# Kernel optimization log

Hardware: AMD Instinct MI355X
Metric: run time of the kernel (lower is better)

## Reference

```python
import jax, jax.numpy as jnp
import numpy as np

B, C, Q, D = 64, 1024, 256, 128
NEG = -1e30  # VERY_NEGATIVE_NUMBER


def setup_inputs() -> dict:
    key = jax.random.key(0)
    k1, k2, k3, k4, k5, k6 = jax.random.split(key, 6)
    return {
        "x_cont": jax.random.normal(k1, (B, C, D), dtype=jnp.float32),
        "x_ques": jax.random.normal(k2, (B, Q, D), dtype=jnp.float32),
        "c_mask": jnp.ones((B, C), dtype=jnp.float32),
        "q_mask": jnp.ones((B, Q), dtype=jnp.float32),
        "W0": jax.random.uniform(k3, (D, 1), jnp.float32, -0.1, 0.1),
        "W1": jax.random.uniform(k4, (D, 1), jnp.float32, -0.1, 0.1),
        "W2": jax.random.uniform(k5, (1, 1, D), jnp.float32, -0.1, 0.1),
        "bias": jnp.zeros((1,), dtype=jnp.float32),
    }


def reference(x_cont, x_ques, c_mask, q_mask, W0, W1, W2, bias):
    # Trilinear similarity S[b,c,q] = x_cont.W0 + x_ques.W1 + (x_cont*W2).x_ques^T + bias
    s0 = x_cont @ W0                                   # [B,C,1]
    s1 = jnp.swapaxes(x_ques @ W1, 1, 2)               # [B,1,Q]
    s2 = jnp.einsum('bcd,bqd->bcq', x_cont * W2, x_ques)  # [B,C,Q]
    S = s0 + s1 + s2 + bias                            # [B,C,Q]

    qm = q_mask[:, None, :]                            # [B,1,Q]
    cm = c_mask[:, :, None]                            # [B,C,1]
    S_ = jax.nn.softmax(S + NEG * (1.0 - qm), axis=-1)           # row softmax [B,C,Q]
    S_T = jnp.swapaxes(jax.nn.softmax(S + NEG * (1.0 - cm), axis=1), 1, 2)  # [B,Q,C]

    c2q = S_ @ x_ques                                  # [B,C,D]
    q2c = (S_ @ S_T) @ x_cont                          # [B,C,D]
    return jnp.concatenate([x_cont, c2q, x_cont * c2q, x_cont * q2c], axis=-1)
```

## Files before the change

### kernel.cpp

```cpp
#include <hip/hip_runtime.h>
#include <math.h>

#define BB 64
#define CC 1024
#define QQ 256
#define DD 128
#define NEGV (-1.0e30f)

typedef short bf8 __attribute__((ext_vector_type(8)));
typedef short bf4 __attribute__((ext_vector_type(4)));
typedef float f4v __attribute__((ext_vector_type(4)));

__device__ __forceinline__ short f2bf(float f) {
    unsigned u = __builtin_bit_cast(unsigned, f);
    u += 0x7FFFu + ((u >> 16) & 1u);
    return (short)(u >> 16);
}
__device__ __forceinline__ float bf2f(short s) {
    unsigned u = ((unsigned)(unsigned short)s) << 16;
    return __builtin_bit_cast(float, u);
}

__global__ __launch_bounds__(256, 2) void k0_all(
        const float* __restrict__ xc, const float* __restrict__ xq,
        const float* __restrict__ W0, const float* __restrict__ W1,
        const float* __restrict__ W2,
        const float* __restrict__ c_mask, const float* __restrict__ q_mask,
        float* __restrict__ s0m, float* __restrict__ s1m,
        short* __restrict__ xc_bf, short* __restrict__ xqw_bf,
        short* __restrict__ xcT_bf, short* __restrict__ xqT_bf) {
    __shared__ float tile[64][129];
    int bid = blockIdx.x;
    const float *src, *W, *mask;
    float* sm; short *rm, *tr;
    int b, tl, R; bool use2;
    if (bid < 1024) {
        b = ((bid >> 7) << 3) | (bid & 7); tl = (bid >> 3) & 15; R = CC;
        src = xc; W = W0; mask = c_mask; sm = s0m; rm = xc_bf; tr = xcT_bf; use2 = false;
    } else {
        int q = bid - 1024;
        b = ((q >> 5) << 3) | (q & 7); tl = (q >> 3) & 3; R = QQ;
        src = xq; W = W1; mask = q_mask; sm = s1m; rm = xqw_bf; tr = xqT_bf; use2 = true;
    }
    int r0 = tl * 64;
    int t = threadIdx.x;
    int c4 = t & 31, rr = t >> 5;
    float4 wv = ((const float4*)W)[c4];
    float4 sc4 = use2 ? ((const float4*)W2)[c4] : make_float4(1.f, 1.f, 1.f, 1.f);
    const float* sb = src + ((size_t)b * R + r0) * DD;
    #pragma unroll
    for (int p = 0; p < 8; ++p) {
        int row = rr + p * 8;
        float4 g = *(const float4*)&sb[(size_t)row * DD + c4 * 4];
        bf4 o;
        o[0] = f2bf(g.x * sc4.x); o[1] = f2bf(g.y * sc4.y);
        o[2] = f2bf(g.z * sc4.z); o[3] = f2bf(g.w * sc4.w);
        *(bf4*)&rm[((size_t)(b * R + r0 + row)) * DD + c4 * 4] = o;
        float part = g.x * wv.x + g.y * wv.y + g.z * wv.z + g.w * wv.w;
        #pragma unroll
        for (int off = 1; off < 32; off <<= 1) part += __shfl_xor(part, off, 64);
        if ((t & 31) == 0)
            sm[(size_t)b * R + r0 + row] =
                part + NEGV * (1.0f - mask[(size_t)b * R + r0 + row]);
        tile[row][c4 * 4 + 0] = g.x; tile[row][c4 * 4 + 1] = g.y;
        tile[row][c4 * 4 + 2] = g.z; tile[row][c4 * 4 + 3] = g.w;
    }
    __syncthreads();
    int rj = (t & 7) * 8;
    #pragma unroll
    for (int pp = 0; pp < 4; ++pp) {
        int d = pp * 32 + (t >> 3);
        bf8 o;
        #pragma unroll
        for (int j = 0; j < 8; ++j) o[j] = f2bf(tile[rj + j][d]);
        *(bf8*)&tr[((size_t)(b * DD + d)) * R + r0 + rj] = o;
    }
}

#define SCP 1032
#define S2P 264
#define XTP 72

#define K1_LDA(G, S, CT)                                                 \
    {                                                                    \
        const short* ar_ = abase + (size_t)(CT) * 64 * DD;               \
        G[0] = *(const bf8*)&ar_[0];  G[1] = *(const bf8*)&ar_[32];      \
        G[2] = *(const bf8*)&ar_[64]; G[3] = *(const bf8*)&ar_[96];      \
        S = *(const f4v*)&s0base[(CT) * 64];                             \
    }

#define K1_STEPA(G, S, CT)                                                            \
    {                                                                                 \
        f4v acc = {0.f, 0.f, 0.f, 0.f};                                               \
        acc = __builtin_amdgcn_mfma_f32_16x16x32_bf16(G[0], bq[0], acc, 0, 0, 0);     \
        acc = __builtin_amdgcn_mfma_f32_16x16x32_bf16(G[1], bq[1], acc, 0, 0, 0);     \
        acc = __builtin_amdgcn_mfma_f32_16x16x32_bf16(G[2], bq[2], acc, 0, 0, 0);     \
        acc = __builtin_amdgcn_mfma_f32_16x16x32_bf16(G[3], bq[3], acc, 0, 0, 0);     \
        bf4 ov;                                                                       \
        ov[0] = f2bf(acc[0] + S[0]); ov[1] = f2bf(acc[1] + S[1]);                     \
        ov[2] = f2bf(acc[2] + S[2]); ov[3] = f2bf(acc[3] + S[3]);                     \
        *(bf4*)&sc[l16][(CT) * 64 + w * 16 + quad * 4] = ov;                          \
        if ((CT) + 4 < 16) K1_LDA(G, S, (CT) + 4);                                    \
    }

#define K1_STG(GS, NXT)                                                  \
    {                                                                    \
        *(bf8*)&xct[dr][c8 * 8] = GS[0];                                 \
        *(bf8*)&xct[dr + 32][c8 * 8] = GS[1];                            \
        *(bf8*)&xct[dr + 64][c8 * 8] = GS[2];                            \
        *(bf8*)&xct[dr + 96][c8 * 8] = GS[3];                            \
        if ((NXT) < 16) {                                                \
            GS[0] = *(const bf8*)&tbase[(NXT) * 64];                     \
            GS[1] = *(const bf8*)&tbase[(size_t)32 * CC + (NXT) * 64];   \
            GS[2] = *(const bf8*)&tbase[(size_t)64 * CC + (NXT) * 64];   \
            GS[3] = *(const bf8*)&tbase[(size_t)96 * CC + (NXT) * 64];   \
        }                                                                \
    }

#define K1_CSTEP(CT)                                                               \
    {                                                                              \
        bf8 a0 = *(const bf8*)&sc[l16][(CT) * 64 + quad * 8];                      \
        bf8 b0 = *(const bf8*)&xct[w * 32 + l16][quad * 8];                        \
        acc0 = __builtin_amdgcn_mfma_f32_16x16x32_bf16(a0, b0, acc0, 0, 0, 0);     \
        bf8 b1 = *(const bf8*)&xct[w * 32 + 16 + l16][quad * 8];                   \
        acc1 = __builtin_amdgcn_mfma_f32_16x16x32_bf16(a0, b1, acc1, 0, 0, 0);     \
        bf8 a1 = *(const bf8*)&sc[l16][(CT) * 64 + 32 + quad * 8];                 \
        bf8 b2 = *(const bf8*)&xct[w * 32 + l16][32 + quad * 8];                   \
        acc0 = __builtin_amdgcn_mfma_f32_16x16x32_bf16(a1, b2, acc0, 0, 0, 0);     \
        bf8 b3 = *(const bf8*)&xct[w * 32 + 16 + l16][32 + quad * 8];              \
        acc1 = __builtin_amdgcn_mfma_f32_16x16x32_bf16(a1, b3, acc1, 0, 0, 0);     \
    }

__global__ __launch_bounds__(256, 3) void k1_colsm(
        const short* __restrict__ xc_bf, const short* __restrict__ xcT_bf,
        const short* __restrict__ xqw_bf, const float* __restrict__ s0m,
        short* __restrict__ AT) {
    __shared__ __align__(16) short sc[16][SCP];
    __shared__ __align__(16) short xct[DD][XTP];
    __shared__ float invl[16];

    int bid = blockIdx.x;
    int qt = (bid >> 3) & 15;
    int b = ((bid >> 7) << 3) | (bid & 7);
    int q0 = qt * 16;
    int t = threadIdx.x, w = t >> 6, l = t & 63;
    int quad = l >> 4, l16 = l & 15;

    bf8 bq[4];
    {
        const short* qp = &xqw_bf[(size_t)(b * QQ + q0 + l16) * DD + quad * 8];
        #pragma unroll
        for (int ks = 0; ks < 4; ++ks) bq[ks] = *(const bf8*)&qp[ks * 32];
    }

    const short* abase = &xc_bf[(size_t)(b * CC + w * 16 + l16) * DD + quad * 8];
    const float* s0base = &s0m[b * CC + w * 16 + quad * 4];
    bf8 gA[4], gB[4], gC[4], gD[4];
    f4v sA, sB, sC, sD;
    K1_LDA(gA, sA, 0); K1_LDA(gB, sB, 1); K1_LDA(gC, sC, 2); K1_LDA(gD, sD, 3);
    #pragma unroll
    for (int c4t = 0; c4t < 16; c4t += 4) {
        K1_STEPA(gA, sA, c4t + 0);
        K1_STEPA(gB, sB, c4t + 1);
        K1_STEPA(gC, sC, c4t + 2);
        K1_STEPA(gD, sD, c4t + 3);
    }

    int c8 = t & 7, dr = t >> 3;
    const short* tbase = &xcT_bf[(size_t)(b * DD + dr) * CC + c8 * 8];
    bf8 gS0[4], gS1[4];
    gS0[0] = *(const bf8*)&tbase[0];
    gS0[1] = *(const bf8*)&tbase[(size_t)32 * CC];
    gS0[2] = *(const bf8*)&tbase[(size_t)64 * CC];
    gS0[3] = *(const bf8*)&tbase[(size_t)96 * CC];
    gS1[0] = *(const bf8*)&tbase[64];
    gS1[1] = *(const bf8*)&tbase[(size_t)32 * CC + 64];
    gS1[2] = *(const bf8*)&tbase[(size_t)64 * CC + 64];
    gS1[3] = *(const bf8*)&tbase[(size_t)96 * CC + 64];

    __syncthreads();

    {
        int q = t >> 4, k = t & 15;
        bf8 v[8];
        #pragma unroll
        for (int j = 0; j < 8; ++j) v[j] = *(const bf8*)&sc[q][k * 8 + j * 128];
        float m = -3.0e38f;
        #pragma unroll
        for (int j = 0; j < 8; ++j)
            #pragma unroll
            for (int e = 0; e < 8; ++e) m = fmaxf(m, bf2f(v[j][e]));
        #pragma unroll
        for (int off = 1; off < 16; off <<= 1) m = fmaxf(m, __shfl_xor(m, off, 64));
        float sum = 0.f;
        #pragma unroll
        for (int j = 0; j < 8; ++j) {
            bf8 o;
            #pragma unroll
            for (int e = 0; e < 8; ++e) {
                float ex = __expf(bf2f(v[j][e]) - m);
                sum += ex;
                o[e] = f2bf(ex);
            }
            *(bf8*)&sc[q][k * 8 + j * 128] = o;
        }
        #pragma unroll
        for (int off = 1; off < 16; off <<= 1) sum += __shfl_xor(sum, off, 64);
        if (k == 0) invl[q] = 1.0f / sum;
    }
    __syncthreads();

    f4v acc0 = {0.f, 0.f, 0.f, 0.f}, acc1 = {0.f, 0.f, 0.f, 0.f};
    #pragma unroll
    for (int ct = 0; ct < 16; ct += 2) {
        K1_STG(gS0, ct + 2);
        __syncthreads();
        K1_CSTEP(ct);
        __syncthreads();
        K1_STG(gS1, ct + 3);
        __syncthreads();
        K1_CSTEP(ct + 1);
        __syncthreads();
    }
    {
        bf4 o0, o1;
        #pragma unroll
        for (int r = 0; r < 4; ++r) {
            float il = invl[quad * 4 + r];
            o0[r] = f2bf(acc0[r] * il);
            o1[r] = f2bf(acc1[r] * il);
        }
        int d0 = w * 32 + l16;
        *(bf4*)&AT[(size_t)(b * DD + d0) * QQ + q0 + quad * 4] = o0;
        *(bf4*)&AT[(size_t)(b * DD + d0 + 16) * QQ + q0 + quad * 4] = o1;
    }
}

#define K2_LDA(G, CT)                                                    \
    {                                                                    \
        const short* ar_ = abase + (size_t)(CT) * 64 * DD;               \
        G[0] = *(const bf8*)&ar_[0];  G[1] = *(const bf8*)&ar_[32];      \
        G[2] = *(const bf8*)&ar_[64]; G[3] = *(const bf8*)&ar_[96];     \
    }

#define K2_STEP1(G, SV, QT)                                                           \
    {                                                                                 \
        f4v acc0 = {0.f, 0.f, 0.f, 0.f}, acc1 = {0.f, 0.f, 0.f, 0.f};                 \
        acc0 = __builtin_amdgcn_mfma_f32_16x16x32_bf16(G[0], bc0[0], acc0, 0, 0, 0);  \
        acc1 = __builtin_amdgcn_mfma_f32_16x16x32_bf16(G[0], bc1[0], acc1, 0, 0, 0);  \
        acc0 = __builtin_amdgcn_mfma_f32_16x16x32_bf16(G[1], bc0[1], acc0, 0, 0, 0);  \
        acc1 = __builtin_amdgcn_mfma_f32_16x16x32_bf16(G[1], bc1[1], acc1, 0, 0, 0);  \
        acc0 = __builtin_amdgcn_mfma_f32_16x16x32_bf16(G[2], bc0[2], acc0, 0, 0, 0);  \
        acc1 = __builtin_amdgcn_mfma_f32_16x16x32_bf16(G[2], bc1[2], acc1, 0, 0, 0);  \
        acc0 = __builtin_amdgcn_mfma_f32_16x16x32_bf16(G[3], bc0[3], acc0, 0, 0, 0);  \
        acc1 = __builtin_amdgcn_mfma_f32_16x16x32_bf16(G[3], bc1[3], acc1, 0, 0, 0);  \
        int qbase_ = (QT) * 64 + w * 16 + quad * 4;                                   \
        bf4 o0, o1;                                                                   \
        o0[0] = f2bf(acc0[0] + SV[0]); o0[1] = f2bf(acc0[1] + SV[1]);                 \
        o0[2] = f2bf(acc0[2] + SV[2]); o0[3] = f2bf(acc0[3] + SV[3]);                 \
        o1[0] = f2bf(acc1[0] + SV[0]); o1[1] = f2bf(acc1[1] + SV[1]);                 \
        o1[2] = f2bf(acc1[2] + SV[2]); o1[3] = f2bf(acc1[3] + SV[3]);                 \
        *(bf4*)&sc2[l16][qbase_] = o0;                                                \
        *(bf4*)&sc2[16 + l16][qbase_] = o1;                                           \
    }

#define K2_SRC(NT) ((NT) < 4 ? (qtb + (size_t)(NT) * 64) : (atb + (size_t)((NT) - 4) * 64))

#define K2_STG(GS, NT)                                                   \
    {                                                                    \
        *(bf8*)&tT[dr][c8 * 8] = GS[0];                                  \
        *(bf8*)&tT[dr + 32][c8 * 8] = GS[1];                             \
        *(bf8*)&tT[dr + 64][c8 * 8] = GS[2];                             \
        *(bf8*)&tT[dr + 96][c8 * 8] = GS[3];                             \
        if ((NT) < 8) {                                                  \
            const short* gs_ = K2_SRC(NT);                               \
            GS[0] = *(const bf8*)&gs_[0];                                \
            GS[1] = *(const bf8*)&gs_[(size_t)32 * QQ];                  \
            GS[2] = *(const bf8*)&gs_[(size_t)64 * QQ];                  \
            GS[3] = *(const bf8*)&gs_[(size_t)96 * QQ];                  \
        }                                                                \
    }

#define K2_CSTEP(TL)                                                                   \
    {                                                                                  \
        int qoff_ = ((TL) & 3) * 64;                                                   \
        _Pragma("unroll")                                                              \
        for (int ks = 0; ks < 2; ++ks) {                                               \
            bf8 a0 = *(const bf8*)&sc2[l16][qoff_ + ks * 32 + quad * 8];               \
            bf8 a1 = *(const bf8*)&sc2[16 + l16][qoff_ + ks * 32 + quad * 8];          \
            bf8 b0 = *(const bf8*)&tT[w * 32 + l16][ks * 32 + quad * 8];               \
            bf8 b1 = *(const bf8*)&tT[w * 32 + 16 + l16][ks * 32 + quad * 8];          \
            if ((TL) < 4) {                                                            \
                ac[0][0] = __builtin_amdgcn_mfma_f32_16x16x32_bf16(a0, b0, ac[0][0], 0, 0, 0); \
                ac[0][1] = __builtin_amdgcn_mfma_f32_16x16x32_bf16(a0, b1, ac[0][1], 0, 0, 0); \
                ac[1][0] = __builtin_amdgcn_mfma_f32_16x16x32_bf16(a1, b0, ac[1][0], 0, 0, 0); \
                ac[1][1] = __builtin_amdgcn_mfma_f32_16x16x32_bf16(a1, b1, ac[1][1], 0, 0, 0); \
            } else {                                                                   \
                aq[0][0] = __builtin_amdgcn_mfma_f32_16x16x32_bf16(a0, b0, aq[0][0], 0, 0, 0); \
                aq[0][1] = __builtin_amdgcn_mfma_f32_16x16x32_bf16(a0, b1, aq[0][1], 0, 0, 0); \
                aq[1][0] = __builtin_amdgcn_mfma_f32_16x16x32_bf16(a1, b0, aq[1][0], 0, 0, 0); \
                aq[1][1] = __builtin_amdgcn_mfma_f32_16x16x32_bf16(a1, b1, aq[1][1], 0, 0, 0); \
            }                                                                          \
        }                                                                              \
    }

__global__ __launch_bounds__(256, 4) void k2_rowsm(
        const float* __restrict__ xc, const short* __restrict__ xc_bf,
        const short* __restrict__ xqw_bf, const short* __restrict__ xqT_bf,
        const short* __restrict__ AT, const float* __restrict__ s1m,
        float* __restrict__ out) {
    __shared__ __align__(16) short sc2[32][S2P];
    __shared__ __align__(16) short tT[DD][XTP];
    __shared__ float invl2[32];

    int bid = blockIdx.x;
    int cb = (bid >> 3) & 31;
    int b = ((bid >> 8) << 3) | (bid & 7);
    int c0g = cb * 32;
    int t = threadIdx.x, w = t >> 6, l = t & 63;
    int quad = l >> 4, l16 = l & 15;

    bf8 bc0[4], bc1[4];
    {
        const short* p0 = &xc_bf[(size_t)(b * CC + c0g + l16) * DD + quad * 8];
        const short* p1 = p0 + 16 * DD;
        #pragma unroll
        for (int ks = 0; ks < 4; ++ks) {
            bc0[ks] = *(const bf8*)&p0[ks * 32];
            bc1[ks] = *(const bf8*)&p1[ks * 32];
        }
    }

    const short* abase = &xqw_bf[(size_t)(b * QQ + w * 16 + l16) * DD + quad * 8];
    const float* s1base = &s1m[b * QQ + w * 16 + quad * 4];
    f4v sv0 = *(const f4v*)&s1base[0];
    f4v sv1 = *(const f4v*)&s1base[64];
    f4v sv2 = *(const f4v*)&s1base[128];
    f4v sv3 = *(const f4v*)&s1base[192];
    bf8 gA[4], gB[4];
    K2_LDA(gA, 0); K2_LDA(gB, 1);
    K2_STEP1(gA, sv0, 0); K2_LDA(gA, 2);
    K2_STEP1(gB, sv1, 1); K2_LDA(gB, 3);
    K2_STEP1(gA, sv2, 2);
    K2_STEP1(gB, sv3, 3);

    int c8 = t & 7, dr = t >> 3;
    const short* qtb = &xqT_bf[(size_t)(b * DD + dr) * QQ + c8 * 8];
    const short* atb = &AT[(size_t)(b * DD + dr) * QQ + c8 * 8];
    bf8 gS0[4], gS1[4];
    gS0[0] = *(const bf8*)&qtb[0];
    gS0[1] = *(const bf8*)&qtb[(size_t)32 * QQ];
    gS0[2] = *(const bf8*)&qtb[(size_t)64 * QQ];
    gS0[3] = *(const bf8*)&qtb[(size_t)96 * QQ];
    gS1[0] = *(const bf8*)&qtb[64];
    gS1[1] = *(const bf8*)&qtb[(size_t)32 * QQ + 64];
    gS1[2] = *(const bf8*)&qtb[(size_t)64 * QQ + 64];
    gS1[3] = *(const bf8*)&qtb[(size_t)96 * QQ + 64];

    __syncthreads();

    {
        int c = t >> 3, k = t & 7;
        bf8 v[4];
        #pragma unroll
        for (int j = 0; j < 4; ++j) v[j] = *(const bf8*)&sc2[c][k * 8 + j * 64];
        float m = -3.0e38f;
        #pragma unroll
        for (int j = 0; j < 4; ++j)
            #pragma unroll
            for (int e = 0; e < 8; ++e) m = fmaxf(m, bf2f(v[j][e]));
        #pragma unroll
        for (int off = 1; off < 8; off <<= 1) m = fmaxf(m, __shfl_xor(m, off, 64));
        float sum = 0.f;
        #pragma unroll
        for (int j = 0; j < 4; ++j) {
            bf8 o;
            #pragma unroll
            for (int e = 0; e < 8; ++e) {
                float ex = __expf(bf2f(v[j][e]) - m);
                sum += ex;
                o[e] = f2bf(ex);
            }
            *(bf8*)&sc2[c][k * 8 + j * 64] = o;
        }
        #pragma unroll
        for (int off = 1; off < 8; off <<= 1) sum += __shfl_xor(sum, off, 64);
        if (k == 0) invl2[c] = 1.0f / sum;
    }
    __syncthreads();

    f4v ac[2][2], aq[2][2];
    f4v zz = {0.f, 0.f, 0.f, 0.f};
    #pragma unroll
    for (int i = 0; i < 2; ++i)
        #pragma unroll
        for (int j = 0; j < 2; ++j) { ac[i][j] = zz; aq[i][j] = zz; }
    #pragma unroll
    for (int tl = 0; tl < 8; tl += 2) {
        K2_STG(gS0, tl + 2);
        __syncthreads();
        K2_CSTEP(tl);
        __syncthreads();
        K2_STG(gS1, tl + 3);
        __syncthreads();
        K2_CSTEP(tl + 1);
        __syncthreads();
    }

    #pragma unroll
    for (int cf = 0; cf < 2; ++cf)
        #pragma unroll
        for (int r = 0; r < 4; ++r) {
            int cl = cf * 16 + quad * 4 + r;
            int c = c0g + cl;
            float il = invl2[cl];
            const float* xrow = xc + (size_t)(b * CC + c) * DD;
            float* orow = out + (size_t)(b * CC + c) * (4 * DD);
            #pragma unroll
            for (int df = 0; df < 2; ++df) {
                int d = w * 32 + df * 16 + l16;
                float xv = xrow[d];
                float c2v = ac[cf][df][r] * il;
                float q2v = aq[cf][df][r] * il;
                orow[d] = xv;
                orow[DD + d] = c2v;
                orow[2 * DD + d] = xv * c2v;
                orow[3 * DD + d] = xv * q2v;
            }
        }
}

extern "C" void kernel_launch(void* const* d_in, const int* in_sizes, int n_in,
                              void* d_out, int out_size, void* d_ws, size_t ws_size,
                              hipStream_t stream) {
    const float* x_cont = (const float*)d_in[0];
    const float* x_ques = (const float*)d_in[1];
    const float* c_mask = (const float*)d_in[2];
    const float* q_mask = (const float*)d_in[3];
    const float* W0     = (const float*)d_in[4];
    const float* W1     = (const float*)d_in[5];
    const float* W2     = (const float*)d_in[6];
    float* out = (float*)d_out;

    char* ws = (char*)d_ws;
    float* s0m    = (float*)ws;  ws += (size_t)BB * CC * 4;
    float* s1m    = (float*)ws;  ws += (size_t)BB * QQ * 4;
    short* xc_bf  = (short*)ws;  ws += (size_t)BB * CC * DD * 2;
    short* xqw_bf = (short*)ws;  ws += (size_t)BB * QQ * DD * 2;
    short* xcT_bf = (short*)ws;  ws += (size_t)BB * CC * DD * 2;
    short* xqT_bf = (short*)ws;  ws += (size_t)BB * QQ * DD * 2;
    short* AT     = (short*)ws;

    k0_all<<<BB * 16 + BB * 4, 256, 0, stream>>>(x_cont, x_ques, W0, W1, W2,
                                                 c_mask, q_mask, s0m, s1m,
                                                 xc_bf, xqw_bf, xcT_bf, xqT_bf);
    k1_colsm<<<BB * 16, 256, 0, stream>>>(xc_bf, xcT_bf, xqw_bf, s0m, AT);
    k2_rowsm<<<BB * 32, 256, 0, stream>>>(x_cont, xc_bf, xqw_bf, xqT_bf, AT, s1m, out);
}
```

Baseline: 261.2 us.

## Use per-wave LDS staging slices and coalesce output stores through LDS

The shared transposed tiles in both kernels are split into per-wave slices of 32 rows, and each wave loads only the rows it later consumes. This removes all block-wide barriers from the inner MFMA loops and relies on in-order LDS access within a wave. The k2 epilogue now stages the c2q and q2c accumulators into reused shared memory, then writes the output with contiguous float4 loads and stores instead of scattered scalar writes. The cost is two extra barriers and an LDS round trip in the epilogue, plus reliance on the reused buffers being large enough.

```diff
diff --git a/kernel.cpp b/kernel.cpp
--- a/kernel.cpp
+++ b/kernel.cpp
@@ -103,31 +103,33 @@
         if ((CT) + 4 < 16) K1_LDA(G, S, (CT) + 4);                                    \
     }
 
-#define K1_STG(GS, NXT)                                                  \
-    {                                                                    \
-        *(bf8*)&xct[dr][c8 * 8] = GS[0];                                 \
-        *(bf8*)&xct[dr + 32][c8 * 8] = GS[1];                            \
-        *(bf8*)&xct[dr + 64][c8 * 8] = GS[2];                            \
-        *(bf8*)&xct[dr + 96][c8 * 8] = GS[3];                            \
-        if ((NXT) < 16) {                                                \
-            GS[0] = *(const bf8*)&tbase[(NXT) * 64];                     \
-            GS[1] = *(const bf8*)&tbase[(size_t)32 * CC + (NXT) * 64];   \
-            GS[2] = *(const bf8*)&tbase[(size_t)64 * CC + (NXT) * 64];   \
-            GS[3] = *(const bf8*)&tbase[(size_t)96 * CC + (NXT) * 64];   \
-        }                                                                \
+#define K1_LDS2(G, CT)                                                   \
+    {                                                                    \
+        G[0] = *(const bf8*)&tbase[(CT) * 64];                           \
+        G[1] = *(const bf8*)&tbase[(size_t)8 * CC + (CT) * 64];          \
+        G[2] = *(const bf8*)&tbase[(size_t)16 * CC + (CT) * 64];         \
+        G[3] = *(const bf8*)&tbase[(size_t)24 * CC + (CT) * 64];         \
+    }
+
+#define K1_WRS2(G)                                                       \
+    {                                                                    \
+        *(bf8*)&xct[w][sr][c8l * 8] = G[0];                              \
+        *(bf8*)&xct[w][sr + 8][c8l * 8] = G[1];                          \
+        *(bf8*)&xct[w][sr + 16][c8l * 8] = G[2];                         \
+        *(bf8*)&xct[w][sr + 24][c8l * 8] = G[3];                         \
     }
 
 #define K1_CSTEP(CT)                                                               \
     {                                                                              \
         bf8 a0 = *(const bf8*)&sc[l16][(CT) * 64 + quad * 8];                      \
-        bf8 b0 = *(const bf8*)&xct[w * 32 + l16][quad * 8];                        \
+        bf8 b0 = *(const bf8*)&xct[w][l16][quad * 8];                              \
         acc0 = __builtin_amdgcn_mfma_f32_16x16x32_bf16(a0, b0, acc0, 0, 0, 0);     \
-        bf8 b1 = *(const bf8*)&xct[w * 32 + 16 + l16][quad * 8];                   \
+        bf8 b1 = *(const bf8*)&xct[w][16 + l16][quad * 8];                         \
         acc1 = __builtin_amdgcn_mfma_f32_16x16x32_bf16(a0, b1, acc1, 0, 0, 0);     \
         bf8 a1 = *(const bf8*)&sc[l16][(CT) * 64 + 32 + quad * 8];                 \
-        bf8 b2 = *(const bf8*)&xct[w * 32 + l16][32 + quad * 8];                   \
+        bf8 b2 = *(const bf8*)&xct[w][l16][32 + quad * 8];                         \
         acc0 = __builtin_amdgcn_mfma_f32_16x16x32_bf16(a1, b2, acc0, 0, 0, 0);     \
-        bf8 b3 = *(const bf8*)&xct[w * 32 + 16 + l16][32 + quad * 8];              \
+        bf8 b3 = *(const bf8*)&xct[w][16 + l16][32 + quad * 8];                    \
         acc1 = __builtin_amdgcn_mfma_f32_16x16x32_bf16(a1, b3, acc1, 0, 0, 0);     \
     }
 
@@ -136,7 +138,7 @@
         const short* __restrict__ xqw_bf, const float* __restrict__ s0m,
         short* __restrict__ AT) {
     __shared__ __align__(16) short sc[16][SCP];
-    __shared__ __align__(16) short xct[DD][XTP];
+    __shared__ __align__(16) short xct[4][32][XTP];
     __shared__ float invl[16];
 
     int bid = blockIdx.x;
@@ -166,17 +168,11 @@
         K1_STEPA(gD, sD, c4t + 3);
     }
 
-    int c8 = t & 7, dr = t >> 3;
-    const short* tbase = &xcT_bf[(size_t)(b * DD + dr) * CC + c8 * 8];
+    int c8l = l & 7, sr = l >> 3;
+    const short* tbase = &xcT_bf[(size_t)(b * DD + w * 32 + sr) * CC + c8l * 8];
     bf8 gS0[4], gS1[4];
-    gS0[0] = *(const bf8*)&tbase[0];
-    gS0[1] = *(const bf8*)&tbase[(size_t)32 * CC];
-    gS0[2] = *(const bf8*)&tbase[(size_t)64 * CC];
-    gS0[3] = *(const bf8*)&tbase[(size_t)96 * CC];
-    gS1[0] = *(const bf8*)&tbase[64];
-    gS1[1] = *(const bf8*)&tbase[(size_t)32 * CC + 64];
-    gS1[2] = *(const bf8*)&tbase[(size_t)64 * CC + 64];
-    gS1[3] = *(const bf8*)&tbase[(size_t)96 * CC + 64];
+    K1_LDS2(gS0, 0);
+    K1_LDS2(gS1, 1);
 
     __syncthreads();
 
@@ -211,16 +207,20 @@
     __syncthreads();
 
     f4v acc0 = {0.f, 0.f, 0.f, 0.f}, acc1 = {0.f, 0.f, 0.f, 0.f};
-    #pragma unroll
-    for (int ct = 0; ct < 16; ct += 2) {
-        K1_STG(gS0, ct + 2);
-        __syncthreads();
+    K1_WRS2(gS0);
+    K1_LDS2(gS0, 2);
+    #pragma unroll
+    for (int ct = 0; ct < 16; ++ct) {
         K1_CSTEP(ct);
-        __syncthreads();
-        K1_STG(gS1, ct + 3);
-        __syncthreads();
-        K1_CSTEP(ct + 1);
-        __syncthreads();
+        if (ct < 15) {
+            if ((ct & 1) == 0) {
+                K1_WRS2(gS1);
+                if (ct + 3 < 16) K1_LDS2(gS1, ct + 3);
+            } else {
+                K1_WRS2(gS0);
+                if (ct + 3 < 16) K1_LDS2(gS0, ct + 3);
+            }
+        }
     }
     {
         bf4 o0, o1;
@@ -240,7 +240,7 @@
     {                                                                    \
         const short* ar_ = abase + (size_t)(CT) * 64 * DD;               \
         G[0] = *(const bf8*)&ar_[0];  G[1] = *(const bf8*)&ar_[32];      \
-        G[2] = *(const bf8*)&ar_[64]; G[3] = *(const bf8*)&ar_[96];     \
+        G[2] = *(const bf8*)&ar_[64]; G[3] = *(const bf8*)&ar_[96];      \
     }
 
 #define K2_STEP1(G, SV, QT)                                                           \
@@ -264,21 +264,23 @@
         *(bf4*)&sc2[16 + l16][qbase_] = o1;                                           \
     }
 
-#define K2_SRC(NT) ((NT) < 4 ? (qtb + (size_t)(NT) * 64) : (atb + (size_t)((NT) - 4) * 64))
-
-#define K2_STG(GS, NT)                                                   \
-    {                                                                    \
-        *(bf8*)&tT[dr][c8 * 8] = GS[0];                                  \
-        *(bf8*)&tT[dr + 32][c8 * 8] = GS[1];                             \
-        *(bf8*)&tT[dr + 64][c8 * 8] = GS[2];                             \
-        *(bf8*)&tT[dr + 96][c8 * 8] = GS[3];                             \
-        if ((NT) < 8) {                                                  \
-            const short* gs_ = K2_SRC(NT);                               \
-            GS[0] = *(const bf8*)&gs_[0];                                \
-            GS[1] = *(const bf8*)&gs_[(size_t)32 * QQ];                  \
-            GS[2] = *(const bf8*)&gs_[(size_t)64 * QQ];                  \
-            GS[3] = *(const bf8*)&gs_[(size_t)96 * QQ];                  \
-        }                                                                \
+#define K2_SRC(NT) ((NT) < 4 ? (qtb + (size_t)((NT) & 3) * 64) : (atb + (size_t)((NT) - 4) * 64))
+
+#define K2_LDS2(G, NT)                                                   \
+    {                                                                    \
+        const short* gs_ = K2_SRC(NT);                                   \
+        G[0] = *(const bf8*)&gs_[0];                                     \
+        G[1] = *(const bf8*)&gs_[(size_t)8 * QQ];                        \
+        G[2] = *(const bf8*)&gs_[(size_t)16 * QQ];                       \
+        G[3] = *(const bf8*)&gs_[(size_t)24 * QQ];                       \
+    }
+
+#define K2_WRS2(G)                                                       \
+    {                                                                    \
+        *(bf8*)&tT[w][sr][c8l * 8] = G[0];                               \
+        *(bf8*)&tT[w][sr + 8][c8l * 8] = G[1];                           \
+        *(bf8*)&tT[w][sr + 16][c8l * 8] = G[2];                          \
+        *(bf8*)&tT[w][sr + 24][c8l * 8] = G[3];                          \
     }
 
 #define K2_CSTEP(TL)                                                                   \
@@ -288,8 +290,8 @@
         for (int ks = 0; ks < 2; ++ks) {                                               \
             bf8 a0 = *(const bf8*)&sc2[l16][qoff_ + ks * 32 + quad * 8];               \
             bf8 a1 = *(const bf8*)&sc2[16 + l16][qoff_ + ks * 32 + quad * 8];          \
-            bf8 b0 = *(const bf8*)&tT[w * 32 + l16][ks * 32 + quad * 8];               \
-            bf8 b1 = *(const bf8*)&tT[w * 32 + 16 + l16][ks * 32 + quad * 8];          \
+            bf8 b0 = *(const bf8*)&tT[w][l16][ks * 32 + quad * 8];                     \
+            bf8 b1 = *(const bf8*)&tT[w][16 + l16][ks * 32 + quad * 8];                \
             if ((TL) < 4) {                                                            \
                 ac[0][0] = __builtin_amdgcn_mfma_f32_16x16x32_bf16(a0, b0, ac[0][0], 0, 0, 0); \
                 ac[0][1] = __builtin_amdgcn_mfma_f32_16x16x32_bf16(a0, b1, ac[0][1], 0, 0, 0); \
@@ -310,7 +312,7 @@
         const short* __restrict__ AT, const float* __restrict__ s1m,
         float* __restrict__ out) {
     __shared__ __align__(16) short sc2[32][S2P];
-    __shared__ __align__(16) short tT[DD][XTP];
+    __shared__ __align__(16) short tT[4][32][XTP];
     __shared__ float invl2[32];
 
     int bid = blockIdx.x;
@@ -344,18 +346,12 @@
     K2_STEP1(gA, sv2, 2);
     K2_STEP1(gB, sv3, 3);
 
-    int c8 = t & 7, dr = t >> 3;
-    const short* qtb = &xqT_bf[(size_t)(b * DD + dr) * QQ + c8 * 8];
-    const short* atb = &AT[(size_t)(b * DD + dr) * QQ + c8 * 8];
+    int c8l = l & 7, sr = l >> 3;
+    const short* qtb = &xqT_bf[(size_t)(b * DD + w * 32 + sr) * QQ + c8l * 8];
+    const short* atb = &AT[(size_t)(b * DD + w * 32 + sr) * QQ + c8l * 8];
     bf8 gS0[4], gS1[4];
-    gS0[0] = *(const bf8*)&qtb[0];
-    gS0[1] = *(const bf8*)&qtb[(size_t)32 * QQ];
-    gS0[2] = *(const bf8*)&qtb[(size_t)64 * QQ];
-    gS0[3] = *(const bf8*)&qtb[(size_t)96 * QQ];
-    gS1[0] = *(const bf8*)&qtb[64];
-    gS1[1] = *(const bf8*)&qtb[(size_t)32 * QQ + 64];
-    gS1[2] = *(const bf8*)&qtb[(size_t)64 * QQ + 64];
-    gS1[3] = *(const bf8*)&qtb[(size_t)96 * QQ + 64];
+    K2_LDS2(gS0, 0);
+    K2_LDS2(gS1, 1);
 
     __syncthreads();
 
@@ -395,39 +391,58 @@
     for (int i = 0; i < 2; ++i)
         #pragma unroll
         for (int j = 0; j < 2; ++j) { ac[i][j] = zz; aq[i][j] = zz; }
-    #pragma unroll
-    for (int tl = 0; tl < 8; tl += 2) {
-        K2_STG(gS0, tl + 2);
-        __syncthreads();
+    K2_WRS2(gS0);
+    K2_LDS2(gS0, 2);
+    #pragma unroll
+    for (int tl = 0; tl < 8; ++tl) {
         K2_CSTEP(tl);
-        __syncthreads();
-        K2_STG(gS1, tl + 3);
-        __syncthreads();
-        K2_CSTEP(tl + 1);
-        __syncthreads();
-    }
-
+        if (tl < 7) {
+            if ((tl & 1) == 0) {
+                K2_WRS2(gS1);
+                if (tl + 3 < 8) K2_LDS2(gS1, tl + 3);
+            } else {
+                K2_WRS2(gS0);
+                if (tl + 3 < 8) K2_LDS2(gS0, tl + 3);
+            }
+        }
+    }
+
+    __syncthreads();
+    float (*c2l)[132] = (float(*)[132])sc2;
+    float (*q2l)[132] = (float(*)[132])tT;
     #pragma unroll
     for (int cf = 0; cf < 2; ++cf)
         #pragma unroll
-        for (int r = 0; r < 4; ++r) {
-            int cl = cf * 16 + quad * 4 + r;
-            int c = c0g + cl;
-            float il = invl2[cl];
-            const float* xrow = xc + (size_t)(b * CC + c) * DD;
-            float* orow = out + (size_t)(b * CC + c) * (4 * DD);
+        for (int df = 0; df < 2; ++df)
             #pragma unroll
-            for (int df = 0; df < 2; ++df) {
+            for (int r = 0; r < 4; ++r) {
+                int cl = cf * 16 + quad * 4 + r;
                 int d = w * 32 + df * 16 + l16;
-                float xv = xrow[d];
-                float c2v = ac[cf][df][r] * il;
-                float q2v = aq[cf][df][r] * il;
-                orow[d] = xv;
-                orow[DD + d] = c2v;
-                orow[2 * DD + d] = xv * c2v;
-                orow[3 * DD + d] = xv * q2v;
+                c2l[cl][d] = ac[cf][df][r];
+                q2l[cl][d] = aq[cf][df][r];
             }
-        }
+    __syncthreads();
+    {
+        int cl = t >> 3, j4 = (t & 7) * 4;
+        float il = invl2[cl];
+        const float* xrow = xc + (size_t)(b * CC + c0g + cl) * DD;
+        float* orow = out + (size_t)(b * CC + c0g + cl) * (4 * DD);
+        #pragma unroll
+        for (int ps = 0; ps < 4; ++ps) {
+            int d = ps * 32 + j4;
+            float4 xv = *(const float4*)&xrow[d];
+            float4 cv = *(const float4*)&c2l[cl][d];
+            float4 qv = *(const float4*)&q2l[cl][d];
+            cv.x *= il; cv.y *= il; cv.z *= il; cv.w *= il;
+            qv.x *= il; qv.y *= il; qv.z *= il; qv.w *= il;
+            *(float4*)&orow[d] = xv;
+            *(float4*)&orow[DD + d] = cv;
+            float4 m2 = make_float4(xv.x * cv.x, xv.y * cv.y, xv.z * cv.z, xv.w * cv.w);
+            *(float4*)&orow[2 * DD + d] = m2;
+            float4 m3 = make_float4(xv.x * qv.x, xv.y * qv.y, xv.z * qv.z, xv.w * qv.w);
+            *(float4*)&orow[3 * DD + d] = m3;
+        }
+    }
 }
 
 extern "C" void kernel_launch(void* const* d_in, const int* in_sizes, int n_in,
```

Result: no change. 258.4 us (-1.1%).
